# Performance work log

Hardware: AMD Instinct MI355X
Metric: run time of the kernel (lower is better)

The kernel has to match this reference:

```python
import jax, jax.numpy as jnp
import numpy as np

B, IN, OUT, COND, N, H = 512, 256, 256, 128, 8, 64
DP = max(1, int(OUT * 0.25))          # 64 periodic units (cos+sin -> 2*DP outputs)
DN = OUT - 2 * DP                     # 128 non-periodic units
TPE = IN * DP + IN * DN + DN          # params per expert
TOTAL = N * TPE


def setup_inputs() -> dict:
    key = jax.random.key(0)
    ks = jax.random.split(key, 16)
    s_in = np.sqrt(2.0 / IN).astype(np.float32)
    inp = {
        "x": jax.random.normal(ks[0], (B, IN), jnp.float32),
        "cond": jax.random.normal(ks[1], (B, COND), jnp.float32),
        # expert base weights (torch: randn * sqrt(2/in))
        "base_wp": jax.random.normal(ks[2], (N, IN, DP), jnp.float32) * s_in,
        "base_wn": jax.random.normal(ks[3], (N, IN, DN), jnp.float32) * s_in,
        "base_bn": jnp.zeros((N, DN), jnp.float32),
        # hypernet: Linear(cond,H) -> ReLU -> Linear(H, TOTAL)
        "hW1": jax.random.normal(ks[4], (COND, H), jnp.float32) / np.sqrt(COND),
        "hb1": jnp.zeros((H,), jnp.float32),
        "hW2": jax.random.normal(ks[5], (H, TOTAL), jnp.float32) / np.sqrt(H),
        "hb2": jnp.zeros((TOTAL,), jnp.float32),
        # gating: Linear(cond,3N) -> ReLU -> Linear(3N, N)
        "gW1": jax.random.normal(ks[6], (COND, 3 * N), jnp.float32) / np.sqrt(COND),
        "gb1": jnp.zeros((3 * N,), jnp.float32),
        "gW2": jax.random.normal(ks[7], (3 * N, N), jnp.float32) / np.sqrt(3 * N),
        "gb2": jnp.zeros((N,), jnp.float32),
    }
    return inp


def reference(x, cond, base_wp, base_wn, base_bn,
              hW1, hb1, hW2, hb2, gW1, gb1, gW2, gb2):
    bsz = x.shape[0]
    # hypernet -> per-sample dynamic deltas
    h = jax.nn.relu(cond @ hW1 + hb1)
    delta = (h @ hW2 + hb2).reshape(bsz, N, TPE)
    d_wp = delta[:, :, : IN * DP].reshape(bsz, N, IN, DP)
    d_wn = delta[:, :, IN * DP: IN * DP + IN * DN].reshape(bsz, N, IN, DN)
    d_bn = delta[:, :, IN * DP + IN * DN:]                  # (B, N, DN)

    # periodic branch: per-sample, per-expert mat-vec then cos/sin
    wp = base_wp[None] + d_wp                                # (B,N,IN,DP)
    per = jnp.einsum('bi,bnip->bnp', x, wp)                  # (B,N,DP)
    per_cos, per_sin = jnp.cos(per), jnp.sin(per)

    # non-periodic branch
    wn = base_wn[None] + d_wn                                # (B,N,IN,DN)
    non = jnp.einsum('bi,bnip->bnp', x, wn) + base_bn[None] + d_bn
    non = jax.nn.relu(non)                                   # (B,N,DN)

    # gating over experts
    logits = jax.nn.relu(cond @ gW1 + gb1) @ gW2 + gb2       # (B,N)
    gw = jax.nn.softmax(logits, axis=1)[:, :, None]          # (B,N,1)

    cos_c = jnp.sum(per_cos * gw, axis=1)
    sin_c = jnp.sum(per_sin * gw, axis=1)
    non_c = jnp.sum(non * gw, axis=1)
    return jnp.concatenate([cos_c, sin_c, non_c], axis=-1)   # (B, 2*DP+DN)
```

## Files before the change

### kernel.cpp

```cpp
#include <hip/hip_runtime.h>
#include <math.h>

#define BB     512
#define INF    256
#define CONDF  128
#define NEXP   8
#define HDIM   64
#define TPE    49280
#define TOTC   394240
#define NSPLIT 16
#define CW     1536
#define KB     261

#define AZ_OFF 0u
#define BT_OFF 17104896u
#define P_OFF  68419584u
#define GW_OFF 93585408u
#define CB_OFF 93601792u

typedef __bf16          bf16x8 __attribute__((ext_vector_type(8)));
typedef unsigned short  us8    __attribute__((ext_vector_type(8)));
typedef float           f32x4  __attribute__((ext_vector_type(4)));

__device__ __forceinline__ unsigned short f2bf(float f) {
  unsigned u = __builtin_bit_cast(unsigned, f);
  u += 0x7fffu + ((u >> 16) & 1u);
  return (unsigned short)(u >> 16);
}
__device__ __forceinline__ float bf2f(unsigned short u) {
  return __builtin_bit_cast(float, ((unsigned)u) << 16);
}

__device__ __forceinline__ void gld16(const void* g, const void* l) {
  __builtin_amdgcn_global_load_lds(
      (const __attribute__((address_space(1))) unsigned int*)g,
      (__attribute__((address_space(3))) unsigned int*)l, 16, 0, 0);
}

__global__ void k_prep(const float* __restrict__ x, const float* __restrict__ cond,
                       const float* __restrict__ hW1, const float* __restrict__ hb1,
                       const float* __restrict__ gW1, const float* __restrict__ gb1,
                       const float* __restrict__ gW2, const float* __restrict__ gb2,
                       unsigned short* __restrict__ Az, float* __restrict__ gw) {
  const int b = blockIdx.x;
  const int tid = threadIdx.x;
  __shared__ float xs[INF], cs[CONDF], hs[HDIM], g1[24], ls[8], es[8];
  xs[tid] = x[b * INF + tid];
  if (tid < CONDF) cs[tid] = cond[b * CONDF + tid];
  __syncthreads();
  if (tid < HDIM) {
    float acc = hb1[tid];
    for (int q = 0; q < CONDF; ++q) acc = fmaf(cs[q], hW1[q * HDIM + tid], acc);
    hs[tid] = fmaxf(acc, 0.f);
  }
  if (tid >= 64 && tid < 88) {
    const int r = tid - 64;
    float acc = gb1[r];
    for (int q = 0; q < CONDF; ++q) acc = fmaf(cs[q], gW1[q * 24 + r], acc);
    g1[r] = fmaxf(acc, 0.f);
  }
  __syncthreads();
  if (tid < NEXP) {
    float acc = gb2[tid];
    for (int j = 0; j < 24; ++j) acc = fmaf(g1[j], gW2[j * NEXP + tid], acc);
    ls[tid] = acc;
  }
  __syncthreads();
  if (tid < NEXP) {
    float m = ls[0];
    for (int j = 1; j < NEXP; ++j) m = fmaxf(m, ls[j]);
    es[tid] = expf(ls[tid] - m);
  }
  __syncthreads();
  if (tid < NEXP) {
    float s = 0.f;
    for (int j = 0; j < NEXP; ++j) s += es[j];
    gw[b * NEXP + tid] = es[tid] / s;
  }
  const int t0 = tid >> 5, ig = tid & 31;
#pragma unroll
  for (int tt = 0; tt < 8; ++tt) {
    const int t = tt * 8 + t0;
    const float hv = hs[t];
    us8 o;
#pragma unroll
    for (int j = 0; j < 8; ++j) o[j] = f2bf(hv * xs[ig * 8 + j]);
    *(us8*)(Az + ((size_t)(t * 4 + (ig >> 3)) * BB + b) * 64 + (ig & 7) * 8) = o;
  }
  Az[((size_t)(256 + (tid >> 6)) * BB + b) * 64 + (tid & 63)] = f2bf(xs[tid]);
  if (tid < HDIM) Az[((size_t)260 * BB + b) * 64 + tid] = f2bf(hs[tid]);
}

__global__ void k_bt(const float* __restrict__ hW2, unsigned short* __restrict__ Bt,
                     const float* __restrict__ bwp, const float* __restrict__ bwn,
                     const float* __restrict__ bbn, const float* __restrict__ hb2,
                     float* __restrict__ colbias) {
  const int bx = blockIdx.x;
  const int t = bx / 24, rem = bx % 24, ne = rem / 3, sec = rem % 3;
  const size_t base = (size_t)t * TOTC + (size_t)ne * TPE + (sec ? 16384 : 0);
  const int dst  = sec ? 128 : 64;
  const int poff = (sec == 2) ? 64 : 0;
  const int cbase = ne * 192 + (sec == 0 ? 0 : (sec == 1 ? 64 : 128));
  const int tid = threadIdx.x;
  __shared__ __align__(16) unsigned short Ls[64 * 256];
#pragma unroll
  for (int it = 0; it < 16; ++it) {
    const int f = it * 256 + tid;
    const int i = f >> 4, p4 = (f & 15) * 4;
    const int e = i >> 3, q = i & 7;
    f32x4 v = *(const f32x4*)(hW2 + base + (size_t)i * dst + poff + p4);
#pragma unroll
    for (int j = 0; j < 4; ++j) {
      const int p = p4 + j;
      Ls[(p << 8) + (((e ^ (p & 31)) << 3) | q)] = f2bf(v[j]);
    }
  }
  if (tid < 64) {
    const int c2 = bx, ne2 = c2 / 192, r2 = c2 % 192;
#pragma unroll
    for (int kb = 0; kb < 5; ++kb) {
      const int j = kb * 64 + tid;
      float v;
      if (j < 256) {
        const int i = j;
        if (r2 < 64) v = bwp[(ne2 * INF + i) * 64 + r2] + hb2[(size_t)ne2 * TPE + i * 64 + r2];
        else         v = bwn[(ne2 * INF + i) * 128 + (r2 - 64)] + hb2[(size_t)ne2 * TPE + 16384 + i * 128 + (r2 - 64)];
      } else {
        const int t2 = j - 256;
        v = (r2 < 64) ? 0.f : hW2[(size_t)t2 * TOTC + (size_t)ne2 * TPE + 49152 + (r2 - 64)];
      }
      Bt[((size_t)(256 + kb) * CW + c2) * 64 + tid] = f2bf(v);
    }
    if (tid == 0)
      colbias[c2] = (r2 < 64) ? 0.f
                  : bbn[ne2 * 128 + (r2 - 64)] + hb2[(size_t)ne2 * TPE + 49152 + (r2 - 64)];
  }
  __syncthreads();
#pragma unroll
  for (int it2 = 0; it2 < 8; ++it2) {
    const int of = it2 * 256 + tid;
    const int p = of >> 5, seg = of & 31, ib = seg >> 3, k8 = seg & 7;
    us8 o = *(const us8*)(&Ls[(p << 8) + ((seg ^ (p & 31)) << 3)]);
    *(us8*)(Bt + ((size_t)(t * 4 + ib) * CW + cbase + p) * 64 + k8 * 8) = o;
  }
}

__launch_bounds__(256, 3)
__global__ void k_gemm(const unsigned short* __restrict__ Az,
                       const unsigned short* __restrict__ Bt,
                       unsigned short* __restrict__ P) {
  const int bid = blockIdx.x;
  const int g  = (bid >> 5) * 8 + (bid & 7);
  const int mt = (bid >> 3) & 3;
  const int nt = g >> 4;
  const int s  = g & 15;
  const int m0 = mt * 128, n0 = nt * 128;
  const int kb0 = s * 16 + (s < 5 ? s : 5);
  const int kb1 = kb0 + 16 + (s < 5 ? 1 : 0);
  const int tid = threadIdx.x;
  __shared__ __align__(16) unsigned short As[128 * 64];
  __shared__ __align__(16) unsigned short Bs[128 * 64];

  f32x4 acc[4][4];
#pragma unroll
  for (int mi = 0; mi < 4; ++mi)
#pragma unroll
    for (int ni = 0; ni < 4; ++ni) acc[mi][ni] = (f32x4){0.f, 0.f, 0.f, 0.f};

  const int wv = tid >> 6, lane = tid & 63;
  const int wm = wv >> 1, wn = wv & 1;
  const int lrow = lane & 15, quad = lane >> 4;
  const int srow = tid >> 3;
  const int sg0  = tid & 7;

  const unsigned short* ab = Az + ((size_t)kb0 * BB + m0) * 64;
  const unsigned short* bb = Bt + ((size_t)kb0 * CW + n0) * 64;

  for (int kb = kb0; kb < kb1; ++kb) {
#pragma unroll
    for (int it = 0; it < 4; ++it) {
      const int r = it * 32 + srow;
      const int ga = sg0 ^ (r & 7);
      const int ldsoff = __builtin_amdgcn_readfirstlane(it * 4096 + wv * 1024);
      gld16(ab + (size_t)r * 64 + ga * 8, (const char*)As + ldsoff);
      gld16(bb + (size_t)r * 64 + ga * 8, (const char*)Bs + ldsoff);
    }
    __syncthreads();
#pragma unroll
    for (int kh = 0; kh < 2; ++kh) {
      bf16x8 af[4], bfr[4];
#pragma unroll
      for (int mi = 0; mi < 4; ++mi) {
        const int r = wm * 64 + mi * 16 + lrow;
        const int ga = (kh * 4 + quad) ^ (r & 7);
        af[mi] = *(const bf16x8*)(As + r * 64 + ga * 8);
      }
#pragma unroll
      for (int ni = 0; ni < 4; ++ni) {
        const int r = wn * 64 + ni * 16 + lrow;
        const int ga = (kh * 4 + quad) ^ (r & 7);
        bfr[ni] = *(const bf16x8*)(Bs + r * 64 + ga * 8);
      }
#pragma unroll
      for (int mi = 0; mi < 4; ++mi)
#pragma unroll
        for (int ni = 0; ni < 4; ++ni)
          acc[mi][ni] = __builtin_amdgcn_mfma_f32_16x16x32_bf16(af[mi], bfr[ni], acc[mi][ni], 0, 0, 0);
    }
    __syncthreads();
    ab += (size_t)BB * 64;
    bb += (size_t)CW * 64;
  }

#pragma unroll
  for (int mi = 0; mi < 4; ++mi) {
    const int row0 = m0 + wm * 64 + mi * 16 + quad * 4;
#pragma unroll
    for (int ni = 0; ni < 4; ++ni) {
      const int col = n0 + wn * 64 + ni * 16 + lrow;
      unsigned short* pp = P + ((size_t)s * BB + row0) * CW + col;
#pragma unroll
      for (int r = 0; r < 4; ++r) pp[(size_t)r * CW] = f2bf(acc[mi][ni][r]);
    }
  }
}

__global__ void k_epi(const unsigned short* __restrict__ P, const float* __restrict__ gw,
                      const float* __restrict__ colbias, float* __restrict__ out) {
  const int b = blockIdx.x;
  const int r = threadIdx.x;
  __shared__ float gws[NEXP];
  if (r < NEXP) gws[r] = gw[b * NEXP + r];
  __syncthreads();
  float co = 0.f, si = 0.f, nc = 0.f;
  for (int n = 0; n < NEXP; ++n) {
    const int c = n * 192 + r;
    float v = colbias[c];
#pragma unroll
    for (int s2 = 0; s2 < NSPLIT; ++s2) v += bf2f(P[((size_t)s2 * BB + b) * CW + c]);
    const float g = gws[n];
    if (r < 64) { co = fmaf(g, cosf(v), co); si = fmaf(g, sinf(v), si); }
    else        { nc = fmaf(g, fmaxf(v, 0.f), nc); }
  }
  if (r < 64) { out[b * 256 + r] = co; out[b * 256 + 64 + r] = si; }
  else        { out[b * 256 + 128 + (r - 64)] = nc; }
}

extern "C" void kernel_launch(void* const* d_in, const int* in_sizes, int n_in,
                              void* d_out, int out_size, void* d_ws, size_t ws_size,
                              hipStream_t stream) {
  const float* x    = (const float*)d_in[0];
  const float* cond = (const float*)d_in[1];
  const float* bwp  = (const float*)d_in[2];
  const float* bwn  = (const float*)d_in[3];
  const float* bbn  = (const float*)d_in[4];
  const float* hW1  = (const float*)d_in[5];
  const float* hb1  = (const float*)d_in[6];
  const float* hW2  = (const float*)d_in[7];
  const float* hb2  = (const float*)d_in[8];
  const float* gW1  = (const float*)d_in[9];
  const float* gb1  = (const float*)d_in[10];
  const float* gW2  = (const float*)d_in[11];
  const float* gb2  = (const float*)d_in[12];
  float* out = (float*)d_out;
  char* ws = (char*)d_ws;

  unsigned short* Az = (unsigned short*)(ws + AZ_OFF);
  unsigned short* Bt = (unsigned short*)(ws + BT_OFF);
  unsigned short* Pp = (unsigned short*)(ws + P_OFF);
  float* gw      = (float*)(ws + GW_OFF);
  float* colbias = (float*)(ws + CB_OFF);

  hipLaunchKernelGGL(k_prep, dim3(BB), dim3(256), 0, stream,
                     x, cond, hW1, hb1, gW1, gb1, gW2, gb2, Az, gw);
  hipLaunchKernelGGL(k_bt, dim3(1536), dim3(256), 0, stream,
                     hW2, Bt, bwp, bwn, bbn, hb2, colbias);
  hipLaunchKernelGGL(k_gemm, dim3(768), dim3(256), 0, stream, Az, Bt, Pp);
  hipLaunchKernelGGL(k_epi, dim3(BB), dim3(192), 0, stream, Pp, gw, colbias, out);
}
```

Measured before the change: 227.1 us.

## Build A operand on the fly in GEMM instead of materializing h⊗x

Measured after the change: 270.7 us. 19.2% more time.

```diff
diff --git a/kernel.cpp b/kernel.cpp
--- a/kernel.cpp
+++ b/kernel.cpp
@@ -1,4 +1,5 @@
 #include <hip/hip_runtime.h>
+#include <hip/hip_bf16.h>
 #include <math.h>
 
 #define BB     512
@@ -12,11 +13,12 @@
 #define CW     1536
 #define KB     261
 
-#define AZ_OFF 0u
-#define BT_OFF 17104896u
-#define P_OFF  68419584u
-#define GW_OFF 93585408u
-#define CB_OFF 93601792u
+#define XB_OFF  0u
+#define HBR_OFF 262144u
+#define GW_OFF  327680u
+#define CB_OFF  344064u
+#define BT_OFF  352256u
+#define P_OFF   51666944u
 
 typedef __bf16          bf16x8 __attribute__((ext_vector_type(8)));
 typedef unsigned short  us8    __attribute__((ext_vector_type(8)));
@@ -37,71 +39,74 @@
       (__attribute__((address_space(3))) unsigned int*)l, 16, 0, 0);
 }
 
-__global__ void k_prep(const float* __restrict__ x, const float* __restrict__ cond,
-                       const float* __restrict__ hW1, const float* __restrict__ hb1,
-                       const float* __restrict__ gW1, const float* __restrict__ gb1,
-                       const float* __restrict__ gW2, const float* __restrict__ gb2,
-                       unsigned short* __restrict__ Az, float* __restrict__ gw) {
-  const int b = blockIdx.x;
-  const int tid = threadIdx.x;
-  __shared__ float xs[INF], cs[CONDF], hs[HDIM], g1[24], ls[8], es[8];
-  xs[tid] = x[b * INF + tid];
-  if (tid < CONDF) cs[tid] = cond[b * CONDF + tid];
-  __syncthreads();
-  if (tid < HDIM) {
-    float acc = hb1[tid];
-    for (int q = 0; q < CONDF; ++q) acc = fmaf(cs[q], hW1[q * HDIM + tid], acc);
-    hs[tid] = fmaxf(acc, 0.f);
-  }
-  if (tid >= 64 && tid < 88) {
-    const int r = tid - 64;
-    float acc = gb1[r];
-    for (int q = 0; q < CONDF; ++q) acc = fmaf(cs[q], gW1[q * 24 + r], acc);
-    g1[r] = fmaxf(acc, 0.f);
-  }
-  __syncthreads();
-  if (tid < NEXP) {
-    float acc = gb2[tid];
-    for (int j = 0; j < 24; ++j) acc = fmaf(g1[j], gW2[j * NEXP + tid], acc);
-    ls[tid] = acc;
-  }
-  __syncthreads();
-  if (tid < NEXP) {
-    float m = ls[0];
-    for (int j = 1; j < NEXP; ++j) m = fmaxf(m, ls[j]);
-    es[tid] = expf(ls[tid] - m);
-  }
-  __syncthreads();
-  if (tid < NEXP) {
-    float s = 0.f;
-    for (int j = 0; j < NEXP; ++j) s += es[j];
-    gw[b * NEXP + tid] = es[tid] / s;
-  }
-  const int t0 = tid >> 5, ig = tid & 31;
-#pragma unroll
-  for (int tt = 0; tt < 8; ++tt) {
-    const int t = tt * 8 + t0;
-    const float hv = hs[t];
-    us8 o;
-#pragma unroll
-    for (int j = 0; j < 8; ++j) o[j] = f2bf(hv * xs[ig * 8 + j]);
-    *(us8*)(Az + ((size_t)(t * 4 + (ig >> 3)) * BB + b) * 64 + (ig & 7) * 8) = o;
-  }
-  Az[((size_t)(256 + (tid >> 6)) * BB + b) * 64 + (tid & 63)] = f2bf(xs[tid]);
-  if (tid < HDIM) Az[((size_t)260 * BB + b) * 64 + tid] = f2bf(hs[tid]);
+__device__ __forceinline__ us8 scale8(us8 xo, unsigned short hb) {
+  union HU { unsigned short u; __hip_bfloat16 b; } hu; hu.u = hb;
+  __hip_bfloat162 h2; h2.x = hu.b; h2.y = hu.b;
+  union VU { us8 u; __hip_bfloat162 h[4]; } a, o;
+  a.u = xo;
+#pragma unroll
+  for (int j = 0; j < 4; ++j) o.h[j] = __hmul2(a.h[j], h2);
+  return o.u;
 }
 
 __global__ void k_bt(const float* __restrict__ hW2, unsigned short* __restrict__ Bt,
                      const float* __restrict__ bwp, const float* __restrict__ bwn,
                      const float* __restrict__ bbn, const float* __restrict__ hb2,
-                     float* __restrict__ colbias) {
+                     float* __restrict__ colbias,
+                     const float* __restrict__ x, const float* __restrict__ cond,
+                     const float* __restrict__ hW1, const float* __restrict__ hb1,
+                     const float* __restrict__ gW1, const float* __restrict__ gb1,
+                     const float* __restrict__ gW2, const float* __restrict__ gb2,
+                     unsigned short* __restrict__ Xb, unsigned short* __restrict__ Hbr,
+                     float* __restrict__ gw) {
   const int bx = blockIdx.x;
+  const int tid = threadIdx.x;
+
+  if (bx >= 1536) {
+    const int b = bx - 1536;
+    __shared__ float xs[INF], cs[CONDF], hs[HDIM], g1[24], ls[8], es[8];
+    xs[tid] = x[b * INF + tid];
+    if (tid < CONDF) cs[tid] = cond[b * CONDF + tid];
+    __syncthreads();
+    if (tid < HDIM) {
+      float acc = hb1[tid];
+      for (int q = 0; q < CONDF; ++q) acc = fmaf(cs[q], hW1[q * HDIM + tid], acc);
+      hs[tid] = fmaxf(acc, 0.f);
+    }
+    if (tid >= 64 && tid < 88) {
+      const int r = tid - 64;
+      float acc = gb1[r];
+      for (int q = 0; q < CONDF; ++q) acc = fmaf(cs[q], gW1[q * 24 + r], acc);
+      g1[r] = fmaxf(acc, 0.f);
+    }
+    __syncthreads();
+    if (tid < NEXP) {
+      float acc = gb2[tid];
+      for (int j = 0; j < 24; ++j) acc = fmaf(g1[j], gW2[j * NEXP + tid], acc);
+      ls[tid] = acc;
+    }
+    __syncthreads();
+    if (tid < NEXP) {
+      float m = ls[0];
+      for (int j = 1; j < NEXP; ++j) m = fmaxf(m, ls[j]);
+      es[tid] = expf(ls[tid] - m);
+    }
+    __syncthreads();
+    if (tid < NEXP) {
+      float s = 0.f;
+      for (int j = 0; j < NEXP; ++j) s += es[j];
+      gw[b * NEXP + tid] = es[tid] / s;
+    }
+    Xb[b * INF + tid] = f2bf(xs[tid]);
+    if (tid < HDIM) Hbr[b * HDIM + tid] = f2bf(hs[tid]);
+    return;
+  }
+
   const int t = bx / 24, rem = bx % 24, ne = rem / 3, sec = rem % 3;
   const size_t base = (size_t)t * TOTC + (size_t)ne * TPE + (sec ? 16384 : 0);
   const int dst  = sec ? 128 : 64;
   const int poff = (sec == 2) ? 64 : 0;
   const int cbase = ne * 192 + (sec == 0 ? 0 : (sec == 1 ? 64 : 128));
-  const int tid = threadIdx.x;
   __shared__ __align__(16) unsigned short Ls[64 * 256];
 #pragma unroll
   for (int it = 0; it < 16; ++it) {
@@ -146,7 +151,8 @@
 }
 
 __launch_bounds__(256, 3)
-__global__ void k_gemm(const unsigned short* __restrict__ Az,
+__global__ void k_gemm(const unsigned short* __restrict__ Xb,
+                       const unsigned short* __restrict__ Hbr,
                        const unsigned short* __restrict__ Bt,
                        unsigned short* __restrict__ P) {
   const int bid = blockIdx.x;
@@ -158,7 +164,6 @@
   const int kb0 = s * 16 + (s < 5 ? s : 5);
   const int kb1 = kb0 + 16 + (s < 5 ? 1 : 0);
   const int tid = threadIdx.x;
-  __shared__ __align__(16) unsigned short As[128 * 64];
   __shared__ __align__(16) unsigned short Bs[128 * 64];
 
   f32x4 acc[4][4];
@@ -172,8 +177,8 @@
   const int lrow = lane & 15, quad = lane >> 4;
   const int srow = tid >> 3;
   const int sg0  = tid & 7;
-
-  const unsigned short* ab = Az + ((size_t)kb0 * BB + m0) * 64;
+  const int arow = m0 + wm * 64 + lrow;
+
   const unsigned short* bb = Bt + ((size_t)kb0 * CW + n0) * 64;
 
   for (int kb = kb0; kb < kb1; ++kb) {
@@ -182,19 +187,32 @@
       const int r = it * 32 + srow;
       const int ga = sg0 ^ (r & 7);
       const int ldsoff = __builtin_amdgcn_readfirstlane(it * 4096 + wv * 1024);
-      gld16(ab + (size_t)r * 64 + ga * 8, (const char*)As + ldsoff);
       gld16(bb + (size_t)r * 64 + ga * 8, (const char*)Bs + ldsoff);
     }
+    bf16x8 af[2][4];
+    {
+      const bool main_kb = (kb < 256);
+      const unsigned short* asrc = (kb < 260) ? (Xb + (kb & 3) * 64) : Hbr;
+      const int astr = (kb < 260) ? INF : HDIM;
+      const int t = kb >> 2;
+#pragma unroll
+      for (int mi = 0; mi < 4; ++mi) {
+        const int row = arow + mi * 16;
+        us8 xo0 = *(const us8*)(asrc + (size_t)row * astr + quad * 8);
+        us8 xo1 = *(const us8*)(asrc + (size_t)row * astr + 32 + quad * 8);
+        if (main_kb) {
+          const unsigned short hb = Hbr[row * HDIM + t];
+          xo0 = scale8(xo0, hb);
+          xo1 = scale8(xo1, hb);
+        }
+        af[0][mi] = *(bf16x8*)&xo0;
+        af[1][mi] = *(bf16x8*)&xo1;
+      }
+    }
     __syncthreads();
 #pragma unroll
     for (int kh = 0; kh < 2; ++kh) {
-      bf16x8 af[4], bfr[4];
-#pragma unroll
-      for (int mi = 0; mi < 4; ++mi) {
-        const int r = wm * 64 + mi * 16 + lrow;
-        const int ga = (kh * 4 + quad) ^ (r & 7);
-        af[mi] = *(const bf16x8*)(As + r * 64 + ga * 8);
-      }
+      bf16x8 bfr[4];
 #pragma unroll
       for (int ni = 0; ni < 4; ++ni) {
         const int r = wn * 64 + ni * 16 + lrow;
@@ -205,10 +223,9 @@
       for (int mi = 0; mi < 4; ++mi)
 #pragma unroll
         for (int ni = 0; ni < 4; ++ni)
-          acc[mi][ni] = __builtin_amdgcn_mfma_f32_16x16x32_bf16(af[mi], bfr[ni], acc[mi][ni], 0, 0, 0);
-    }
-    __syncthreads();
-    ab += (size_t)BB * 64;
+          acc[mi][ni] = __builtin_amdgcn_mfma_f32_16x16x32_bf16(af[kh][mi], bfr[ni], acc[mi][ni], 0, 0, 0);
+    }
+    __syncthreads();
     bb += (size_t)CW * 64;
   }
 
@@ -265,16 +282,16 @@
   float* out = (float*)d_out;
   char* ws = (char*)d_ws;
 
-  unsigned short* Az = (unsigned short*)(ws + AZ_OFF);
+  unsigned short* Xb  = (unsigned short*)(ws + XB_OFF);
+  unsigned short* Hbr = (unsigned short*)(ws + HBR_OFF);
+  float* gw      = (float*)(ws + GW_OFF);
+  float* colbias = (float*)(ws + CB_OFF);
   unsigned short* Bt = (unsigned short*)(ws + BT_OFF);
   unsigned short* Pp = (unsigned short*)(ws + P_OFF);
-  float* gw      = (float*)(ws + GW_OFF);
-  float* colbias = (float*)(ws + CB_OFF);
-
-  hipLaunchKernelGGL(k_prep, dim3(BB), dim3(256), 0, stream,
-                     x, cond, hW1, hb1, gW1, gb1, gW2, gb2, Az, gw);
-  hipLaunchKernelGGL(k_bt, dim3(1536), dim3(256), 0, stream,
-                     hW2, Bt, bwp, bwn, bbn, hb2, colbias);
-  hipLaunchKernelGGL(k_gemm, dim3(768), dim3(256), 0, stream, Az, Bt, Pp);
+
+  hipLaunchKernelGGL(k_bt, dim3(2048), dim3(256), 0, stream,
+                     hW2, Bt, bwp, bwn, bbn, hb2, colbias,
+                     x, cond, hW1, hb1, gW1, gb1, gW2, gb2, Xb, Hbr, gw);
+  hipLaunchKernelGGL(k_gemm, dim3(768), dim3(256), 0, stream, Xb, Hbr, Bt, Pp);
   hipLaunchKernelGGL(k_epi, dim3(BB), dim3(192), 0, stream, Pp, gw, colbias, out);
 }
```
